# Kernel optimization log

Hardware: AMD Instinct MI355X
Metric: run time of the kernel (lower is better)

The kernel has to match this reference:

```python
import jax, jax.numpy as jnp
import numpy as np
import math

B, T, C, H = 4, 4096, 1024, 16
D = C // H

def setup_inputs() -> dict:
    key = jax.random.key(0)
    k1, k2, k3, k4, k5 = jax.random.split(key, 5)
    s = 1.0 / math.sqrt(C)
    return {
        "x": jax.random.normal(k1, (B, T, C), dtype=jnp.float32),
        "W_qkv": jax.random.normal(k2, (C, 3 * C), dtype=jnp.float32) * s,
        "b_qkv": jax.random.normal(k3, (3 * C,), dtype=jnp.float32) * 0.01,
        "W_out": jax.random.normal(k4, (C, C), dtype=jnp.float32) * s,
        "b_out": jax.random.normal(k5, (C,), dtype=jnp.float32) * 0.01,
    }

def reference(x, W_qkv, b_qkv, W_out, b_out):
    qkv = x @ W_qkv + b_qkv                      # (B,T,3C)
    q, k, v = jnp.split(qkv, 3, axis=2)
    q = q.reshape(B, T, H, D)
    k = k.reshape(B, T, H, D)
    v = v.reshape(B, T, H, D)
    # attention over the HEAD axis per (B,T): scores (B,T,H,H)
    att = jnp.einsum('bthd,btgd->bthg', q, k) / math.sqrt(D)
    att = jax.nn.softmax(att, axis=-1)
    out = jnp.einsum('bthg,btgd->bthd', att, v)  # (B,T,H,D)
    out = out.reshape(B, T, C)
    return out @ W_out + b_out
```

## Files before the change

kernel.cpp:

```cpp
#include <hip/hip_runtime.h>
#include <cstdint>
#include <cstddef>

constexpr int Bc = 4;
constexpr int Tc = 4096;
constexpr int Cc = 1024;
constexpr int Hc = 16;
constexpr int Dc = 64;
constexpr int Mc = Bc * Tc;
constexpr int N1c = 3 * Cc;
constexpr int Kc = Cc;

typedef __bf16 bf16x8 __attribute__((ext_vector_type(8)));
typedef float  f32x4  __attribute__((ext_vector_type(4)));
typedef __attribute__((address_space(1))) uint32_t gu32;
typedef __attribute__((address_space(3))) uint32_t lu32;

__device__ __forceinline__ float bf2f(unsigned short u) {
    return __uint_as_float(((unsigned)u) << 16);
}
__device__ __forceinline__ unsigned short f2bf(float f) {
    unsigned u = __float_as_uint(f);
    u += 0x7FFF + ((u >> 16) & 1);
    return (unsigned short)(u >> 16);
}

__device__ __forceinline__ void load_lds16(const void* g, void* l) {
    __builtin_amdgcn_global_load_lds((gu32*)(uintptr_t)g, (lu32*)(uintptr_t)l, 16, 0, 0);
}

__global__ void convert_bf16_kernel(const float* __restrict__ in,
                                    unsigned short* __restrict__ out, int n) {
    int i = (blockIdx.x * blockDim.x + threadIdx.x) * 4;
    if (i >= n) return;
    float4 v = *(const float4*)(in + i);
    *(ushort4*)(out + i) = make_ushort4(f2bf(v.x), f2bf(v.y), f2bf(v.z), f2bf(v.w));
}

__global__ void transpose_convert_kernel(const float* __restrict__ W,
                                         unsigned short* __restrict__ Wt,
                                         int K, int N) {
    __shared__ float tile[32][33];
    int n0 = blockIdx.x * 32, k0 = blockIdx.y * 32;
    for (int i = threadIdx.y; i < 32; i += 8)
        tile[i][threadIdx.x] = W[(size_t)(k0 + i) * N + n0 + threadIdx.x];
    __syncthreads();
    for (int i = threadIdx.y; i < 32; i += 8)
        Wt[(size_t)(n0 + i) * K + k0 + threadIdx.x] = f2bf(tile[threadIdx.x][i]);
}

template <bool OUT_BF16>
__global__ __launch_bounds__(256) void gemm_bt_kernel(
    const unsigned short* __restrict__ A,
    const unsigned short* __restrict__ Bt,
    const float* __restrict__ bias,
    void* __restrict__ Cout,
    int M, int N, int K) {
    __shared__ unsigned short sA[128 * 32];
    __shared__ unsigned short sB[128 * 32];
    const int tid  = threadIdx.x;
    const int w    = tid >> 6;
    const int lane = tid & 63;
    const int m0 = blockIdx.y * 128;
    const int n0 = blockIdx.x * 128;

    const int lr = lane >> 2;
    const int lc = (lane & 3) * 8;
    const unsigned short* gA0 = A  + (size_t)(m0 + w * 32      + lr) * K + lc;
    const unsigned short* gA1 = A  + (size_t)(m0 + w * 32 + 16 + lr) * K + lc;
    const unsigned short* gB0 = Bt + (size_t)(n0 + w * 32      + lr) * K + lc;
    const unsigned short* gB1 = Bt + (size_t)(n0 + w * 32 + 16 + lr) * K + lc;
    unsigned short* lA0 = sA + (w * 32     ) * 32;
    unsigned short* lA1 = sA + (w * 32 + 16) * 32;
    unsigned short* lB0 = sB + (w * 32     ) * 32;
    unsigned short* lB1 = sB + (w * 32 + 16) * 32;

    const int wm = (w >> 1) * 64;
    const int wn = (w & 1) * 64;
    const int fr = lane & 15;
    const int fq = lane >> 4;
    const unsigned short* aP = sA + (wm + fr) * 32 + fq * 8;
    const unsigned short* bP = sB + (wn + fr) * 32 + fq * 8;

    const f32x4 zero4 = {0.f, 0.f, 0.f, 0.f};
    f32x4 acc[4][4];
    for (int i = 0; i < 4; ++i)
        for (int j = 0; j < 4; ++j) acc[i][j] = zero4;

    for (int kt = 0; kt < K; kt += 32) {
        load_lds16(gA0, lA0);
        load_lds16(gA1, lA1);
        load_lds16(gB0, lB0);
        load_lds16(gB1, lB1);
        gA0 += 32; gA1 += 32; gB0 += 32; gB1 += 32;
        __syncthreads();

        bf16x8 af[4], bfr[4];
        #pragma unroll
        for (int mi = 0; mi < 4; ++mi) af[mi]  = *(const bf16x8*)(aP + mi * 16 * 32);
        #pragma unroll
        for (int ni = 0; ni < 4; ++ni) bfr[ni] = *(const bf16x8*)(bP + ni * 16 * 32);
        #pragma unroll
        for (int mi = 0; mi < 4; ++mi)
            #pragma unroll
            for (int ni = 0; ni < 4; ++ni)
                acc[mi][ni] = __builtin_amdgcn_mfma_f32_16x16x32_bf16(
                    af[mi], bfr[ni], acc[mi][ni], 0, 0, 0);
        __syncthreads();
    }

    #pragma unroll
    for (int mi = 0; mi < 4; ++mi) {
        #pragma unroll
        for (int ni = 0; ni < 4; ++ni) {
            int row = m0 + wm + mi * 16 + fq * 4;
            int col = n0 + wn + ni * 16 + fr;
            float bb = bias[col];
            #pragma unroll
            for (int r = 0; r < 4; ++r) {
                float v = acc[mi][ni][r] + bb;
                if (OUT_BF16)
                    ((unsigned short*)Cout)[(size_t)(row + r) * N + col] = f2bf(v);
                else
                    ((float*)Cout)[(size_t)(row + r) * N + col] = v;
            }
        }
    }
}

__global__ __launch_bounds__(256) void attn_mfma_kernel(
    const unsigned short* __restrict__ qkv,
    unsigned short* __restrict__ att) {
    __shared__ char smem[4 * 3584];
    const int w    = threadIdx.x >> 6;
    const int lane = threadIdx.x & 63;
    const int m    = lane & 15;
    const int q    = lane >> 4;
    const int row  = blockIdx.x * 4 + w;
    unsigned short* sV = (unsigned short*)(smem + w * 3584);
    float*          sP = (float*)(smem + w * 3584 + 2304);

    const unsigned short* src = qkv + (size_t)row * 3072;

    bf16x8 aq0 = *(const bf16x8*)(src + m * 64 + q * 8);
    bf16x8 aq1 = *(const bf16x8*)(src + m * 64 + 32 + q * 8);
    bf16x8 bk0 = *(const bf16x8*)(src + 1024 + m * 64 + q * 8);
    bf16x8 bk1 = *(const bf16x8*)(src + 1024 + m * 64 + 32 + q * 8);

    #pragma unroll
    for (int t = 0; t < 2; ++t) {
        int G = t * 64 + lane;
        int r = G >> 3, p = G & 7;
        *(uint4*)(sV + r * 72 + p * 8) = *(const uint4*)(src + 2048 + G * 8);
    }

    f32x4 s = {0.f, 0.f, 0.f, 0.f};
    s = __builtin_amdgcn_mfma_f32_16x16x32_bf16(aq0, bk0, s, 0, 0, 0);
    s = __builtin_amdgcn_mfma_f32_16x16x32_bf16(aq1, bk1, s, 0, 0, 0);

    #pragma unroll
    for (int r = 0; r < 4; ++r) {
        float t0 = s[r] * 0.125f;
        float mx = t0;
        mx = fmaxf(mx, __shfl_xor(mx, 1));
        mx = fmaxf(mx, __shfl_xor(mx, 2));
        mx = fmaxf(mx, __shfl_xor(mx, 4));
        mx = fmaxf(mx, __shfl_xor(mx, 8));
        float e = __expf(t0 - mx);
        float su = e;
        su += __shfl_xor(su, 1);
        su += __shfl_xor(su, 2);
        su += __shfl_xor(su, 4);
        su += __shfl_xor(su, 8);
        sP[(q * 4 + r) * 20 + m] = e / su;
    }
    __syncthreads();

    const float* pr = sP + m * 20 + (q & 1) * 8;
    float4 pf0 = *(const float4*)(pr);
    float4 pf1 = *(const float4*)(pr + 4);
    const bool act = (q < 2);
    union { unsigned short u[8]; bf16x8 b; } pa;
    pa.u[0] = act ? f2bf(pf0.x) : 0;
    pa.u[1] = act ? f2bf(pf0.y) : 0;
    pa.u[2] = act ? f2bf(pf0.z) : 0;
    pa.u[3] = act ? f2bf(pf0.w) : 0;
    pa.u[4] = act ? f2bf(pf1.x) : 0;
    pa.u[5] = act ? f2bf(pf1.y) : 0;
    pa.u[6] = act ? f2bf(pf1.z) : 0;
    pa.u[7] = act ? f2bf(pf1.w) : 0;

    const unsigned short* vb = sV + (q & 1) * 8 * 72;
    unsigned short* dst = att + (size_t)row * 1024;
    #pragma unroll
    for (int c4 = 0; c4 < 4; ++c4) {
        union { unsigned short u[8]; bf16x8 b; } vf;
        #pragma unroll
        for (int j = 0; j < 8; ++j) vf.u[j] = vb[j * 72 + c4 * 16 + m];
        f32x4 o = {0.f, 0.f, 0.f, 0.f};
        o = __builtin_amdgcn_mfma_f32_16x16x32_bf16(pa.b, vf.b, o, 0, 0, 0);
        #pragma unroll
        for (int r = 0; r < 4; ++r)
            dst[(q * 4 + r) * 64 + c4 * 16 + m] = f2bf(o[r]);
    }
}

extern "C" void kernel_launch(void* const* d_in, const int* in_sizes, int n_in,
                              void* d_out, int out_size, void* d_ws, size_t ws_size,
                              hipStream_t stream) {
    const float* x    = (const float*)d_in[0];
    const float* Wqkv = (const float*)d_in[1];
    const float* bqkv = (const float*)d_in[2];
    const float* Wout = (const float*)d_in[3];
    const float* bout = (const float*)d_in[4];
    float* out = (float*)d_out;

    char* ws = (char*)d_ws;
    unsigned short* xb   = (unsigned short*)ws;                 ws += (size_t)Mc * Kc * 2;
    unsigned short* Wqkt = (unsigned short*)ws;                 ws += (size_t)N1c * Kc * 2;
    unsigned short* Wot  = (unsigned short*)ws;                 ws += (size_t)Cc * Kc * 2;
    unsigned short* qkv  = (unsigned short*)ws;
    unsigned short* att  = xb;

    convert_bf16_kernel<<<(Mc * Kc) / 4 / 256, 256, 0, stream>>>(x, xb, Mc * Kc);
    transpose_convert_kernel<<<dim3(N1c / 32, Kc / 32), dim3(32, 8), 0, stream>>>(Wqkv, Wqkt, Kc, N1c);
    transpose_convert_kernel<<<dim3(Cc / 32, Kc / 32), dim3(32, 8), 0, stream>>>(Wout, Wot, Kc, Cc);
    gemm_bt_kernel<true><<<dim3(N1c / 128, Mc / 128), 256, 0, stream>>>(xb, Wqkt, bqkv, qkv, Mc, N1c, Kc);
    attn_mfma_kernel<<<Mc / 4, 256, 0, stream>>>(qkv, att);
    gemm_bt_kernel<false><<<dim3(Cc / 128, Mc / 128), 256, 0, stream>>>(att, Wot, bout, out, Mc, Cc, Kc);
}
```

Baseline: 358.3 us.

## Pre-pack GEMM operands into MFMA fragment tiles and load directly to registers

```diff
diff --git a/kernel.cpp b/kernel.cpp
--- a/kernel.cpp
+++ b/kernel.cpp
@@ -10,11 +10,10 @@
 constexpr int Mc = Bc * Tc;
 constexpr int N1c = 3 * Cc;
 constexpr int Kc = Cc;
+constexpr int KBc = Kc / 32;
 
 typedef __bf16 bf16x8 __attribute__((ext_vector_type(8)));
 typedef float  f32x4  __attribute__((ext_vector_type(4)));
-typedef __attribute__((address_space(1))) uint32_t gu32;
-typedef __attribute__((address_space(3))) uint32_t lu32;
 
 __device__ __forceinline__ float bf2f(unsigned short u) {
     return __uint_as_float(((unsigned)u) << 16);
@@ -25,90 +24,107 @@
     return (unsigned short)(u >> 16);
 }
 
-__device__ __forceinline__ void load_lds16(const void* g, void* l) {
-    __builtin_amdgcn_global_load_lds((gu32*)(uintptr_t)g, (lu32*)(uintptr_t)l, 16, 0, 0);
-}
-
-__global__ void convert_bf16_kernel(const float* __restrict__ in,
-                                    unsigned short* __restrict__ out, int n) {
-    int i = (blockIdx.x * blockDim.x + threadIdx.x) * 4;
-    if (i >= n) return;
-    float4 v = *(const float4*)(in + i);
-    *(ushort4*)(out + i) = make_ushort4(f2bf(v.x), f2bf(v.y), f2bf(v.z), f2bf(v.w));
-}
-
-__global__ void transpose_convert_kernel(const float* __restrict__ W,
-                                         unsigned short* __restrict__ Wt,
+
+__global__ void convert_x_packed(const float* __restrict__ x,
+                                 unsigned short* __restrict__ Ap) {
+    const int w = threadIdx.x >> 6, lane = threadIdx.x & 63;
+    const int t = blockIdx.x * 4 + w;
+    const int mb = t >> 5, kb = t & 31;
+    const int r = lane >> 2, c = lane & 3;
+    const float* src = x + (size_t)(mb * 16 + r) * Kc + kb * 32 + c * 8;
+    float4 f0 = *(const float4*)src;
+    float4 f1 = *(const float4*)(src + 4);
+    unsigned short u[8];
+    u[0] = f2bf(f0.x); u[1] = f2bf(f0.y); u[2] = f2bf(f0.z); u[3] = f2bf(f0.w);
+    u[4] = f2bf(f1.x); u[5] = f2bf(f1.y); u[6] = f2bf(f1.z); u[7] = f2bf(f1.w);
+    *(uint4*)(Ap + (size_t)t * 512 + (c * 16 + r) * 8) = *(uint4*)u;
+}
+
+__global__ void transpose_convert_packed(const float* __restrict__ W,
+                                         unsigned short* __restrict__ Bp,
                                          int K, int N) {
     __shared__ float tile[32][33];
-    int n0 = blockIdx.x * 32, k0 = blockIdx.y * 32;
-    for (int i = threadIdx.y; i < 32; i += 8)
-        tile[i][threadIdx.x] = W[(size_t)(k0 + i) * N + n0 + threadIdx.x];
+    const int tx = threadIdx.x, ty = threadIdx.y;
+    const int n0 = blockIdx.x * 32, k0 = blockIdx.y * 32;
+    for (int i = ty; i < 32; i += 8)
+        tile[i][tx] = W[(size_t)(k0 + i) * N + n0 + tx];
     __syncthreads();
-    for (int i = threadIdx.y; i < 32; i += 8)
-        Wt[(size_t)(n0 + i) * K + k0 + threadIdx.x] = f2bf(tile[threadIdx.x][i]);
+    const int t = ty * 32 + tx;
+    const int h = t >> 7, rr = t & 127, lane = rr >> 1, half = rr & 1;
+    const int fq = lane >> 4, fn = lane & 15;
+    unsigned short u[4];
+    #pragma unroll
+    for (int j = 0; j < 4; ++j)
+        u[j] = f2bf(tile[fq * 8 + half * 4 + j][h * 16 + fn]);
+    size_t tileIdx = (size_t)((n0 >> 4) + h) * (K >> 5) + (k0 >> 5);
+    *(uint2*)(Bp + tileIdx * 512 + lane * 8 + half * 4) = *(uint2*)u;
 }
 
 template <bool OUT_BF16>
-__global__ __launch_bounds__(256) void gemm_bt_kernel(
-    const unsigned short* __restrict__ A,
-    const unsigned short* __restrict__ Bt,
+__global__ __launch_bounds__(256, 3) void flat_gemm_kernel(
+    const unsigned short* __restrict__ Ap,
+    const unsigned short* __restrict__ Bp,
     const float* __restrict__ bias,
     void* __restrict__ Cout,
     int M, int N, int K) {
-    __shared__ unsigned short sA[128 * 32];
-    __shared__ unsigned short sB[128 * 32];
-    const int tid  = threadIdx.x;
-    const int w    = tid >> 6;
-    const int lane = tid & 63;
+    const int KB = K >> 5;
+    const int w    = threadIdx.x >> 6;
+    const int lane = threadIdx.x & 63;
     const int m0 = blockIdx.y * 128;
     const int n0 = blockIdx.x * 128;
-
-    const int lr = lane >> 2;
-    const int lc = (lane & 3) * 8;
-    const unsigned short* gA0 = A  + (size_t)(m0 + w * 32      + lr) * K + lc;
-    const unsigned short* gA1 = A  + (size_t)(m0 + w * 32 + 16 + lr) * K + lc;
-    const unsigned short* gB0 = Bt + (size_t)(n0 + w * 32      + lr) * K + lc;
-    const unsigned short* gB1 = Bt + (size_t)(n0 + w * 32 + 16 + lr) * K + lc;
-    unsigned short* lA0 = sA + (w * 32     ) * 32;
-    unsigned short* lA1 = sA + (w * 32 + 16) * 32;
-    unsigned short* lB0 = sB + (w * 32     ) * 32;
-    unsigned short* lB1 = sB + (w * 32 + 16) * 32;
-
     const int wm = (w >> 1) * 64;
     const int wn = (w & 1) * 64;
+
+    const unsigned short* Abase = Ap + (size_t)(((m0 + wm) >> 4) * KB) * 512 + lane * 8;
+    const unsigned short* Bbase = Bp + (size_t)(((n0 + wn) >> 4) * KB) * 512 + lane * 8;
+    const int miStride = KB * 512;
+    const int kbStride = 512;
+
+    const f32x4 zero4 = {0.f, 0.f, 0.f, 0.f};
+    f32x4 acc[4][4];
+    #pragma unroll
+    for (int i = 0; i < 4; ++i)
+        #pragma unroll
+        for (int j = 0; j < 4; ++j) acc[i][j] = zero4;
+
+    bf16x8 a0[4], b0[4], a1[4], b1[4];
+    #pragma unroll
+    for (int mi = 0; mi < 4; ++mi) a0[mi] = *(const bf16x8*)(Abase + mi * miStride);
+    #pragma unroll
+    for (int ni = 0; ni < 4; ++ni) b0[ni] = *(const bf16x8*)(Bbase + ni * miStride);
+
+    #pragma unroll 1
+    for (int kb = 0; kb < KB; kb += 2) {
+        #pragma unroll
+        for (int mi = 0; mi < 4; ++mi)
+            a1[mi] = *(const bf16x8*)(Abase + mi * miStride + (kb + 1) * kbStride);
+        #pragma unroll
+        for (int ni = 0; ni < 4; ++ni)
+            b1[ni] = *(const bf16x8*)(Bbase + ni * miStride + (kb + 1) * kbStride);
+        #pragma unroll
+        for (int mi = 0; mi < 4; ++mi)
+            #pragma unroll
+            for (int ni = 0; ni < 4; ++ni)
+                acc[mi][ni] = __builtin_amdgcn_mfma_f32_16x16x32_bf16(
+                    a0[mi], b0[ni], acc[mi][ni], 0, 0, 0);
+        if (kb + 2 < KB) {
+            #pragma unroll
+            for (int mi = 0; mi < 4; ++mi)
+                a0[mi] = *(const bf16x8*)(Abase + mi * miStride + (kb + 2) * kbStride);
+            #pragma unroll
+            for (int ni = 0; ni < 4; ++ni)
+                b0[ni] = *(const bf16x8*)(Bbase + ni * miStride + (kb + 2) * kbStride);
+        }
+        #pragma unroll
+        for (int mi = 0; mi < 4; ++mi)
+            #pragma unroll
+            for (int ni = 0; ni < 4; ++ni)
+                acc[mi][ni] = __builtin_amdgcn_mfma_f32_16x16x32_bf16(
+                    a1[mi], b1[ni], acc[mi][ni], 0, 0, 0);
+    }
+
     const int fr = lane & 15;
     const int fq = lane >> 4;
-    const unsigned short* aP = sA + (wm + fr) * 32 + fq * 8;
-    const unsigned short* bP = sB + (wn + fr) * 32 + fq * 8;
-
-    const f32x4 zero4 = {0.f, 0.f, 0.f, 0.f};
-    f32x4 acc[4][4];
-    for (int i = 0; i < 4; ++i)
-        for (int j = 0; j < 4; ++j) acc[i][j] = zero4;
-
-    for (int kt = 0; kt < K; kt += 32) {
-        load_lds16(gA0, lA0);
-        load_lds16(gA1, lA1);
-        load_lds16(gB0, lB0);
-        load_lds16(gB1, lB1);
-        gA0 += 32; gA1 += 32; gB0 += 32; gB1 += 32;
-        __syncthreads();
-
-        bf16x8 af[4], bfr[4];
-        #pragma unroll
-        for (int mi = 0; mi < 4; ++mi) af[mi]  = *(const bf16x8*)(aP + mi * 16 * 32);
-        #pragma unroll
-        for (int ni = 0; ni < 4; ++ni) bfr[ni] = *(const bf16x8*)(bP + ni * 16 * 32);
-        #pragma unroll
-        for (int mi = 0; mi < 4; ++mi)
-            #pragma unroll
-            for (int ni = 0; ni < 4; ++ni)
-                acc[mi][ni] = __builtin_amdgcn_mfma_f32_16x16x32_bf16(
-                    af[mi], bfr[ni], acc[mi][ni], 0, 0, 0);
-        __syncthreads();
-    }
-
     #pragma unroll
     for (int mi = 0; mi < 4; ++mi) {
         #pragma unroll
@@ -130,7 +146,7 @@
 
 __global__ __launch_bounds__(256) void attn_mfma_kernel(
     const unsigned short* __restrict__ qkv,
-    unsigned short* __restrict__ att) {
+    unsigned short* __restrict__ attP) {
     __shared__ char smem[4 * 3584];
     const int w    = threadIdx.x >> 6;
     const int lane = threadIdx.x & 63;
@@ -191,7 +207,8 @@
     pa.u[7] = act ? f2bf(pf1.w) : 0;
 
     const unsigned short* vb = sV + (q & 1) * 8 * 72;
-    unsigned short* dst = att + (size_t)row * 1024;
+    const size_t tileBase = (size_t)(row >> 4) * 32 * 512;
+    const int fr_tok = row & 15;
     #pragma unroll
     for (int c4 = 0; c4 < 4; ++c4) {
         union { unsigned short u[8]; bf16x8 b; } vf;
@@ -200,8 +217,12 @@
         f32x4 o = {0.f, 0.f, 0.f, 0.f};
         o = __builtin_amdgcn_mfma_f32_16x16x32_bf16(pa.b, vf.b, o, 0, 0, 0);
         #pragma unroll
-        for (int r = 0; r < 4; ++r)
-            dst[(q * 4 + r) * 64 + c4 * 16 + m] = f2bf(o[r]);
+        for (int r = 0; r < 4; ++r) {
+            int col = (q * 4 + r) * 64 + c4 * 16 + m;
+            size_t off = tileBase + (size_t)(col >> 5) * 512
+                       + (((col >> 3) & 3) * 16 + fr_tok) * 8 + (col & 7);
+            attP[off] = f2bf(o[r]);
+        }
     }
 }
 
@@ -216,16 +237,16 @@
     float* out = (float*)d_out;
 
     char* ws = (char*)d_ws;
-    unsigned short* xb   = (unsigned short*)ws;                 ws += (size_t)Mc * Kc * 2;
-    unsigned short* Wqkt = (unsigned short*)ws;                 ws += (size_t)N1c * Kc * 2;
-    unsigned short* Wot  = (unsigned short*)ws;                 ws += (size_t)Cc * Kc * 2;
+    unsigned short* xp   = (unsigned short*)ws;                 ws += (size_t)Mc * Kc * 2;
+    unsigned short* Wqkp = (unsigned short*)ws;                 ws += (size_t)N1c * Kc * 2;
+    unsigned short* Wop  = (unsigned short*)ws;                 ws += (size_t)Cc * Kc * 2;
     unsigned short* qkv  = (unsigned short*)ws;
-    unsigned short* att  = xb;
-
-    convert_bf16_kernel<<<(Mc * Kc) / 4 / 256, 256, 0, stream>>>(x, xb, Mc * Kc);
-    transpose_convert_kernel<<<dim3(N1c / 32, Kc / 32), dim3(32, 8), 0, stream>>>(Wqkv, Wqkt, Kc, N1c);
-    transpose_convert_kernel<<<dim3(Cc / 32, Kc / 32), dim3(32, 8), 0, stream>>>(Wout, Wot, Kc, Cc);
-    gemm_bt_kernel<true><<<dim3(N1c / 128, Mc / 128), 256, 0, stream>>>(xb, Wqkt, bqkv, qkv, Mc, N1c, Kc);
-    attn_mfma_kernel<<<Mc / 4, 256, 0, stream>>>(qkv, att);
-    gemm_bt_kernel<false><<<dim3(Cc / 128, Mc / 128), 256, 0, stream>>>(att, Wot, bout, out, Mc, Cc, Kc);
-}
+    unsigned short* attP = xp;
+
+    convert_x_packed<<<(Mc / 16) * KBc / 4, 256, 0, stream>>>(x, xp);
+    transpose_convert_packed<<<dim3(N1c / 32, Kc / 32), dim3(32, 8), 0, stream>>>(Wqkv, Wqkp, Kc, N1c);
+    transpose_convert_packed<<<dim3(Cc / 32, Kc / 32), dim3(32, 8), 0, stream>>>(Wout, Wop, Kc, Cc);
+    flat_gemm_kernel<true><<<dim3(N1c / 128, Mc / 128), 256, 0, stream>>>(xp, Wqkp, bqkv, qkv, Mc, N1c, Kc);
+    attn_mfma_kernel<<<Mc / 4, 256, 0, stream>>>(qkv, attP);
+    flat_gemm_kernel<false><<<dim3(Cc / 128, Mc / 128), 256, 0, stream>>>(attP, Wop, bout, out, Mc, Cc, Kc);
+}
```

Result: faster. 336.8 us (-6.0%).
